# Kernel tuning notes

Hardware: AMD Instinct MI355X
Metric: run time of the kernel (lower is better)

The kernel has to match this reference:

```python
import jax, jax.numpy as jnp
import numpy as np
from jax import lax

NUM_CLASSES = 5
N_ITER = 3
IC = 32 * 14 * 14  # 6272 primary capsules
IN_DIM = 14
OUT_DIM = 1


def squash(s):
    # s: [B, N, D]; squash along capsule dim D (dim=2 in torch code)
    sq = jnp.sum(s * s, axis=2)
    scale = sq / (1.0 + sq) / jnp.sqrt(sq)
    return s * scale[:, :, None]


def setup_inputs() -> dict:
    key = jax.random.key(0)
    ks = jax.random.split(key, 7)
    B = 1024
    inp = jax.random.normal(ks[0], (B, 1, 59, 59), dtype=jnp.float32)
    # conv1: Conv2d(1, 32, k=5, s=2)
    W1 = jax.random.normal(ks[1], (32, 1, 5, 5), dtype=jnp.float32) * 0.1
    b1 = jax.random.normal(ks[2], (32,), dtype=jnp.float32) * 0.01
    # primary caps conv: Conv2d(32, 32*14, k=1, s=2) -> 1x1 kernel stored as [448,32]
    Wp = jax.random.normal(ks[3], (32 * 14, 32), dtype=jnp.float32) * 0.1
    bp = jax.random.normal(ks[4], (32 * 14,), dtype=jnp.float32) * 0.01
    # digit caps transform weights: [input_caps, input_dim, output_caps*output_dim]
    stdv = 1.0 / np.sqrt(IC)
    caps_W = jax.random.uniform(ks[5], (IC, IN_DIM, NUM_CLASSES * OUT_DIM), dtype=jnp.float32,
                                minval=-stdv, maxval=stdv)
    # routing logits (learned, initialized zero in torch)
    b_route = jnp.zeros((IC, NUM_CLASSES), dtype=jnp.float32)
    return {"input": inp, "r": 3, "W1": W1, "b1": b1, "Wp": Wp, "bp": bp,
            "caps_W": caps_W, "b_route": b_route}


def _forward(inp, W1, b1, Wp, bp, caps_W, b_route):
    B = inp.shape[0]
    # conv1 + relu: [B,32,28,28]
    x = lax.conv_general_dilated(inp, W1, window_strides=(2, 2), padding="VALID",
                                 dimension_numbers=("NCHW", "OIHW", "NCHW"))
    x = jax.nn.relu(x + b1[None, :, None, None])
    # primary caps: 1x1 conv with stride 2 == strided slice + channel matmul
    xs = x[:, :, ::2, ::2]  # [B,32,14,14]
    pc = jnp.einsum("oc,bchw->bohw", Wp, xs) + bp[None, :, None, None]  # [B,448,14,14]
    pc = pc.reshape(B, 32, 14, 14, 14)          # [B, caps, dim, H, W]
    pc = jnp.transpose(pc, (0, 1, 3, 4, 2))     # [B, caps, H, W, dim]
    pc = pc.reshape(B, IC, IN_DIM)              # [B, 6272, 14]
    pc = squash(pc)
    # digit caps predictions: u_predict [B, IC, OC, OD]
    u = jnp.einsum("bni,nio->bno", pc, caps_W).reshape(B, IC, NUM_CLASSES, OUT_DIM)
    # routing by agreement
    c = jax.nn.softmax(b_route, axis=1)                     # [IC, OC]
    s = jnp.einsum("io,biod->bod", c, u)                    # [B, OC, OD]
    v = squash(s)
    b_batch = jnp.broadcast_to(b_route, (B, IC, NUM_CLASSES))
    for _ in range(N_ITER):
        b_batch = b_batch + jnp.sum(u * v[:, None, :, :], axis=-1)
        c = jax.nn.softmax(b_batch, axis=2)                 # [B, IC, OC]
        s = jnp.einsum("bio,biod->bod", c, u)
        v = squash(s)
    # class probabilities = capsule lengths: [B, OC]
    return jnp.sqrt(jnp.sum(v * v, axis=2))


def reference(input, r, W1, b1, Wp, bp, caps_W, b_route):
    # r is accepted but unused, matching the torch forward signature
    return _forward(input, W1, b1, Wp, bp, caps_W, b_route)
```

## Files before the change

kernel.cpp:

```cpp
#include <hip/hip_runtime.h>
#include <math.h>


#define NTH    512
#define NWAVES 8
#define IC     6272
#define NCLS   5

__global__ __launch_bounds__(NTH, 1)
void caps_fused(const float* __restrict__ inp,
                const float* __restrict__ W1,
                const float* __restrict__ b1,
                const float* __restrict__ Wp,
                const float* __restrict__ bp,
                const float* __restrict__ capsW,
                const float* __restrict__ broute,
                float* __restrict__ out)
{
    extern __shared__ float lds[];
    float* s_xs  = lds;
    float* s_W1  = s_xs + 6272;
    float* s_b1  = s_W1 + 800;
    float* s_bp  = s_b1 + 32;
    float* s_red = s_bp + 448;
    float* s_v   = s_red + 40;
    float* s_u   = s_v + 8;
    float* s_in  = s_u;

    const int b    = blockIdx.x;
    const int tid  = threadIdx.x;
    const int lane = tid & 63;
    const int wv   = tid >> 6;

    const float* inb = inp + (size_t)b * (59 * 59);
    for (int i = tid; i < 59 * 59; i += NTH) s_in[i] = inb[i];
    for (int i = tid; i < 800;     i += NTH) s_W1[i] = W1[i];
    if (tid < 32) s_b1[tid] = b1[tid];
    for (int i = tid; i < 448;     i += NTH) s_bp[i] = bp[i];
    __syncthreads();

    for (int n = tid; n < IC; n += NTH) {
        const int c  = n / 196;
        const int hw = n - c * 196;
        const int h  = hw / 14;
        const int w  = hw - h * 14;
        const float* ip = s_in + (4 * h) * 59 + 4 * w;
        const float* wk = s_W1 + c * 25;
        float acc = s_b1[c];
        #pragma unroll
        for (int kh = 0; kh < 5; ++kh)
            #pragma unroll
            for (int kw = 0; kw < 5; ++kw)
                acc = fmaf(ip[kh * 59 + kw], wk[kh * 5 + kw], acc);
        s_xs[n] = fmaxf(acc, 0.0f);
    }
    __syncthreads();

    for (int gi = 0; gi < 4; ++gi) {
        const int g = wv + gi * NWAVES;
        float pc0[14], pc1[14], pc2[14], pc3[14];
        #pragma unroll
        for (int i = 0; i < 14; ++i) { pc0[i] = 0.f; pc1[i] = 0.f; pc2[i] = 0.f; pc3[i] = 0.f; }
        const float* wpg = Wp + (size_t)g * (14 * 32);
        for (int c = 0; c < 32; ++c) {
            const float* xc = s_xs + c * 196;
            const float x0 = xc[lane];
            const float x1 = xc[64 + lane];
            const float x2 = xc[128 + lane];
            const float x3 = xc[192 + (lane & 3)];
            #pragma unroll
            for (int i = 0; i < 14; ++i) {
                const float w = wpg[i * 32 + c];
                pc0[i] = fmaf(w, x0, pc0[i]);
                pc1[i] = fmaf(w, x1, pc1[i]);
                pc2[i] = fmaf(w, x2, pc2[i]);
                pc3[i] = fmaf(w, x3, pc3[i]);
            }
        }
        auto emit = [&](float* pc, int r) {
            const int hw = r * 64 + lane;
            if (hw < 196) {
                const int n = g * 196 + hw;
                float sq = 0.f;
                #pragma unroll
                for (int i = 0; i < 14; ++i) {
                    pc[i] += s_bp[g * 14 + i];
                    sq = fmaf(pc[i], pc[i], sq);
                }
                const float scale = sq / (1.0f + sq) / sqrtf(sq);
                float uo[5] = {0.f, 0.f, 0.f, 0.f, 0.f};
                const float* cw = capsW + (size_t)n * 70;
                #pragma unroll
                for (int i = 0; i < 14; ++i) {
                    const float p = pc[i] * scale;
                    #pragma unroll
                    for (int o = 0; o < 5; ++o)
                        uo[o] = fmaf(p, cw[i * 5 + o], uo[o]);
                }
                #pragma unroll
                for (int o = 0; o < 5; ++o) s_u[n * 5 + o] = uo[o];
            }
        };
        emit(pc0, 0); emit(pc1, 1); emit(pc2, 2); emit(pc3, 3);
    }
    __syncthreads();

    float V[5] = {0.f, 0.f, 0.f, 0.f, 0.f};
    for (int it = 0; it < 4; ++it) {
        float sacc[5] = {0.f, 0.f, 0.f, 0.f, 0.f};
        for (int n = tid; n < IC; n += NTH) {
            const float* br = broute + (size_t)n * 5;
            float uu[5], l[5];
            #pragma unroll
            for (int o = 0; o < 5; ++o) {
                uu[o] = s_u[n * 5 + o];
                l[o]  = fmaf(uu[o], V[o], br[o]);
            }
            const float m = fmaxf(fmaxf(fmaxf(l[0], l[1]), fmaxf(l[2], l[3])), l[4]);
            float e[5], es = 0.f;
            #pragma unroll
            for (int o = 0; o < 5; ++o) { e[o] = __expf(l[o] - m); es += e[o]; }
            const float inv = 1.0f / es;
            #pragma unroll
            for (int o = 0; o < 5; ++o)
                sacc[o] = fmaf(uu[o], e[o] * inv, sacc[o]);
        }
        #pragma unroll
        for (int off = 32; off > 0; off >>= 1)
            #pragma unroll
            for (int o = 0; o < 5; ++o)
                sacc[o] += __shfl_down(sacc[o], off);
        if (lane == 0) {
            #pragma unroll
            for (int o = 0; o < 5; ++o) s_red[wv * 5 + o] = sacc[o];
        }
        __syncthreads();
        if (tid == 0) {
            #pragma unroll
            for (int o = 0; o < 5; ++o) {
                float s = 0.f;
                for (int w2 = 0; w2 < NWAVES; ++w2) s += s_red[w2 * 5 + o];
                s_v[o] = s * fabsf(s) / (1.0f + s * s);
            }
        }
        __syncthreads();
        #pragma unroll
        for (int o = 0; o < 5; ++o) V[o] += s_v[o];
    }

    if (tid < NCLS) out[b * NCLS + tid] = fabsf(s_v[tid]);
}

extern "C" void kernel_launch(void* const* d_in, const int* in_sizes, int n_in,
                              void* d_out, int out_size, void* d_ws, size_t ws_size,
                              hipStream_t stream)
{
    const float* inp   = (const float*)d_in[0];
    const float* W1    = (const float*)d_in[2];
    const float* b1    = (const float*)d_in[3];
    const float* Wp    = (const float*)d_in[4];
    const float* bp    = (const float*)d_in[5];
    const float* capsW = (const float*)d_in[6];
    const float* brt   = (const float*)d_in[7];
    float* out = (float*)d_out;

    const int B = in_sizes[0] / (59 * 59);
    const size_t lds_bytes = (size_t)(6272 + 800 + 32 + 448 + 40 + 8 + 31360) * sizeof(float);
    (void)hipFuncSetAttribute((const void*)caps_fused,
                              hipFuncAttributeMaxDynamicSharedMemorySize,
                              (int)lds_bytes);
    caps_fused<<<B, NTH, lds_bytes, stream>>>(inp, W1, b1, Wp, bp, capsW, brt, out);
}
```

Measured before the change: 618.5 us.

## Keep capsule predictions in registers, stage Wp in LDS, double threads

Doubles the block to 1024 threads (16 waves) so each wave handles two capsule groups instead of four. The per-capsule prediction vectors u stay in registers across the routing iterations rather than going through a large LDS buffer. This shrinks LDS use from about 155KB to about 73KB, which could let more than one block share a CU. Wp slices are staged into LDS in a transposed layout instead of being read per lane from global memory, and the squash scale is simplified algebraically. The cost is heavier register pressure from holding 40 u values per thread at a 1024-thread launch bound, which risks spilling.

```diff
diff --git a/kernel.cpp b/kernel.cpp
--- a/kernel.cpp
+++ b/kernel.cpp
@@ -2,12 +2,12 @@
 #include <math.h>
 
 
-#define NTH    512
-#define NWAVES 8
+#define NTH    1024
+#define NW     16
 #define IC     6272
 #define NCLS   5
 
-__global__ __launch_bounds__(NTH, 1)
+__global__ __launch_bounds__(NTH)
 void caps_fused(const float* __restrict__ inp,
                 const float* __restrict__ W1,
                 const float* __restrict__ b1,
@@ -18,14 +18,14 @@
                 float* __restrict__ out)
 {
     extern __shared__ float lds[];
-    float* s_xs  = lds;
-    float* s_W1  = s_xs + 6272;
+    float* s_in  = lds;
+    float* s_W1  = s_in + 3481;
     float* s_b1  = s_W1 + 800;
     float* s_bp  = s_b1 + 32;
-    float* s_red = s_bp + 448;
-    float* s_v   = s_red + 40;
-    float* s_u   = s_v + 8;
-    float* s_in  = s_u;
+    float* s_xs  = s_bp + 448;
+    float* s_wp  = s_xs + 6272;
+    float* s_red = s_wp + 7168;
+    float* s_v   = s_red + 80;
 
     const int b    = blockIdx.x;
     const int tid  = threadIdx.x;
@@ -36,7 +36,7 @@
     for (int i = tid; i < 59 * 59; i += NTH) s_in[i] = inb[i];
     for (int i = tid; i < 800;     i += NTH) s_W1[i] = W1[i];
     if (tid < 32) s_b1[tid] = b1[tid];
-    for (int i = tid; i < 448;     i += NTH) s_bp[i] = bp[i];
+    if (tid < 448) s_bp[tid] = bp[tid];
     __syncthreads();
 
     for (int n = tid; n < IC; n += NTH) {
@@ -54,98 +54,120 @@
                 acc = fmaf(ip[kh * 59 + kw], wk[kh * 5 + kw], acc);
         s_xs[n] = fmaxf(acc, 0.0f);
     }
-    __syncthreads();
 
-    for (int gi = 0; gi < 4; ++gi) {
-        const int g = wv + gi * NWAVES;
+    float u[2][4][NCLS];
+
+    #pragma unroll
+    for (int gi = 0; gi < 2; ++gi) {
+        __syncthreads();
+        for (int idx = tid; idx < 16 * 448; idx += NTH) {
+            const int c     = idx & 31;
+            const int i     = (idx >> 5) % 14;
+            const int slice = idx / 448;
+            s_wp[slice * 448 + c * 14 + i] = Wp[(size_t)(slice + gi * 16) * 448 + i * 32 + c];
+        }
+        __syncthreads();
+
+        const int g = wv + gi * 16;
+        const float* wpb = s_wp + wv * 448;
         float pc0[14], pc1[14], pc2[14], pc3[14];
         #pragma unroll
-        for (int i = 0; i < 14; ++i) { pc0[i] = 0.f; pc1[i] = 0.f; pc2[i] = 0.f; pc3[i] = 0.f; }
-        const float* wpg = Wp + (size_t)g * (14 * 32);
+        for (int i = 0; i < 14; ++i) {
+            const float bias = s_bp[g * 14 + i];
+            pc0[i] = bias; pc1[i] = bias; pc2[i] = bias; pc3[i] = bias;
+        }
         for (int c = 0; c < 32; ++c) {
             const float* xc = s_xs + c * 196;
             const float x0 = xc[lane];
             const float x1 = xc[64 + lane];
             const float x2 = xc[128 + lane];
             const float x3 = xc[192 + (lane & 3)];
+            const float* wc = wpb + c * 14;
             #pragma unroll
             for (int i = 0; i < 14; ++i) {
-                const float w = wpg[i * 32 + c];
+                const float w = wc[i];
                 pc0[i] = fmaf(w, x0, pc0[i]);
                 pc1[i] = fmaf(w, x1, pc1[i]);
                 pc2[i] = fmaf(w, x2, pc2[i]);
                 pc3[i] = fmaf(w, x3, pc3[i]);
             }
         }
-        auto emit = [&](float* pc, int r) {
-            const int hw = r * 64 + lane;
-            if (hw < 196) {
-                const int n = g * 196 + hw;
-                float sq = 0.f;
-                #pragma unroll
-                for (int i = 0; i < 14; ++i) {
-                    pc[i] += s_bp[g * 14 + i];
-                    sq = fmaf(pc[i], pc[i], sq);
-                }
-                const float scale = sq / (1.0f + sq) / sqrtf(sq);
-                float uo[5] = {0.f, 0.f, 0.f, 0.f, 0.f};
-                const float* cw = capsW + (size_t)n * 70;
-                #pragma unroll
-                for (int i = 0; i < 14; ++i) {
-                    const float p = pc[i] * scale;
-                    #pragma unroll
-                    for (int o = 0; o < 5; ++o)
-                        uo[o] = fmaf(p, cw[i * 5 + o], uo[o]);
-                }
-                #pragma unroll
-                for (int o = 0; o < 5; ++o) s_u[n * 5 + o] = uo[o];
-            }
-        };
-        emit(pc0, 0); emit(pc1, 1); emit(pc2, 2); emit(pc3, 3);
+
+        #define EMIT(PC, R)                                                     \
+        {                                                                       \
+            const int hw = (R) * 64 + lane;                                     \
+            if (hw < 196) {                                                     \
+                const int n = g * 196 + hw;                                     \
+                float sq = 0.f;                                                 \
+                _Pragma("unroll")                                               \
+                for (int i = 0; i < 14; ++i) sq = fmaf(PC[i], PC[i], sq);       \
+                const float scale = sqrtf(sq) / (1.0f + sq);                    \
+                float uo[NCLS] = {0.f, 0.f, 0.f, 0.f, 0.f};                     \
+                const float* cw = capsW + (size_t)n * 70;                       \
+                _Pragma("unroll")                                               \
+                for (int i = 0; i < 14; ++i) {                                  \
+                    const float p = PC[i] * scale;                              \
+                    _Pragma("unroll")                                           \
+                    for (int o = 0; o < NCLS; ++o)                              \
+                        uo[o] = fmaf(p, cw[i * 5 + o], uo[o]);                  \
+                }                                                               \
+                _Pragma("unroll")                                               \
+                for (int o = 0; o < NCLS; ++o) u[gi][R][o] = uo[o];             \
+            } else {                                                            \
+                _Pragma("unroll")                                               \
+                for (int o = 0; o < NCLS; ++o) u[gi][R][o] = 0.f;               \
+            }                                                                   \
+        }
+        EMIT(pc0, 0) EMIT(pc1, 1) EMIT(pc2, 2) EMIT(pc3, 3)
+        #undef EMIT
     }
     __syncthreads();
 
-    float V[5] = {0.f, 0.f, 0.f, 0.f, 0.f};
+    float V[NCLS] = {0.f, 0.f, 0.f, 0.f, 0.f};
     for (int it = 0; it < 4; ++it) {
-        float sacc[5] = {0.f, 0.f, 0.f, 0.f, 0.f};
-        for (int n = tid; n < IC; n += NTH) {
-            const float* br = broute + (size_t)n * 5;
-            float uu[5], l[5];
+        float sacc[NCLS] = {0.f, 0.f, 0.f, 0.f, 0.f};
+        #pragma unroll
+        for (int gi = 0; gi < 2; ++gi) {
+            const int g = wv + gi * 16;
             #pragma unroll
-            for (int o = 0; o < 5; ++o) {
-                uu[o] = s_u[n * 5 + o];
-                l[o]  = fmaf(uu[o], V[o], br[o]);
+            for (int r = 0; r < 4; ++r) {
+                const int hw = r * 64 + lane;
+                if (hw < 196) {
+                    const int n = g * 196 + hw;
+                    const float* br = broute + (size_t)n * 5;
+                    float l[NCLS];
+                    #pragma unroll
+                    for (int o = 0; o < NCLS; ++o)
+                        l[o] = fmaf(u[gi][r][o], V[o], br[o]);
+                    const float m = fmaxf(fmaxf(fmaxf(l[0], l[1]), fmaxf(l[2], l[3])), l[4]);
+                    float e[NCLS], es = 0.f;
+                    #pragma unroll
+                    for (int o = 0; o < NCLS; ++o) { e[o] = __expf(l[o] - m); es += e[o]; }
+                    const float inv = 1.0f / es;
+                    #pragma unroll
+                    for (int o = 0; o < NCLS; ++o)
+                        sacc[o] = fmaf(u[gi][r][o], e[o] * inv, sacc[o]);
+                }
             }
-            const float m = fmaxf(fmaxf(fmaxf(l[0], l[1]), fmaxf(l[2], l[3])), l[4]);
-            float e[5], es = 0.f;
-            #pragma unroll
-            for (int o = 0; o < 5; ++o) { e[o] = __expf(l[o] - m); es += e[o]; }
-            const float inv = 1.0f / es;
-            #pragma unroll
-            for (int o = 0; o < 5; ++o)
-                sacc[o] = fmaf(uu[o], e[o] * inv, sacc[o]);
         }
         #pragma unroll
         for (int off = 32; off > 0; off >>= 1)
             #pragma unroll
-            for (int o = 0; o < 5; ++o)
+            for (int o = 0; o < NCLS; ++o)
                 sacc[o] += __shfl_down(sacc[o], off);
         if (lane == 0) {
             #pragma unroll
-            for (int o = 0; o < 5; ++o) s_red[wv * 5 + o] = sacc[o];
+            for (int o = 0; o < NCLS; ++o) s_red[wv * 5 + o] = sacc[o];
         }
         __syncthreads();
-        if (tid == 0) {
-            #pragma unroll
-            for (int o = 0; o < 5; ++o) {
-                float s = 0.f;
-                for (int w2 = 0; w2 < NWAVES; ++w2) s += s_red[w2 * 5 + o];
-                s_v[o] = s * fabsf(s) / (1.0f + s * s);
-            }
+        if (tid < NCLS) {
+            float s = 0.f;
+            for (int w2 = 0; w2 < NW; ++w2) s += s_red[w2 * 5 + tid];
+            s_v[tid] = s * fabsf(s) / (1.0f + s * s);
         }
         __syncthreads();
         #pragma unroll
-        for (int o = 0; o < 5; ++o) V[o] += s_v[o];
+        for (int o = 0; o < NCLS; ++o) V[o] += s_v[o];
     }
 
     if (tid < NCLS) out[b * NCLS + tid] = fabsf(s_v[tid]);
@@ -165,7 +187,7 @@
     float* out = (float*)d_out;
 
     const int B = in_sizes[0] / (59 * 59);
-    const size_t lds_bytes = (size_t)(6272 + 800 + 32 + 448 + 40 + 8 + 31360) * sizeof(float);
+    const size_t lds_bytes = (size_t)(3481 + 800 + 32 + 448 + 6272 + 7168 + 80 + 8) * sizeof(float);
     (void)hipFuncSetAttribute((const void*)caps_fused,
                               hipFuncAttributeMaxDynamicSharedMemorySize,
                               (int)lds_bytes);
```

Result: slower. 1.573 ms (+154.3%).

## Transpose xs to swizzled HW-major layout and vectorize primary-caps matmul loads

Applied to the files above, without the earlier changes.

Stores the conv1 output as [hw][32 channels] with an XOR swizzle so each lane can load all 32 channels for its position with float4 LDS reads without bank conflicts. The primary-caps matmul now loops over positions in pairs, holding 32 inputs in registers, and reads Wp and bias with a wave-uniform (readfirstlane) base so they can become scalar loads. It also drops the LDS bias copy and simplifies the squash scale to sqrt(sq)/(1+sq). This aims to cut LDS traffic and per-channel global weight loads, but raises register pressure (64 input values plus 28 accumulators) and could cause spills.

```diff
diff --git a/kernel.cpp b/kernel.cpp
--- a/kernel.cpp
+++ b/kernel.cpp
@@ -21,8 +21,7 @@
     float* s_xs  = lds;
     float* s_W1  = s_xs + 6272;
     float* s_b1  = s_W1 + 800;
-    float* s_bp  = s_b1 + 32;
-    float* s_red = s_bp + 448;
+    float* s_red = s_b1 + 32;
     float* s_v   = s_red + 40;
     float* s_u   = s_v + 8;
     float* s_in  = s_u;
@@ -31,12 +30,12 @@
     const int tid  = threadIdx.x;
     const int lane = tid & 63;
     const int wv   = tid >> 6;
+    const int wvs  = __builtin_amdgcn_readfirstlane(wv);
 
     const float* inb = inp + (size_t)b * (59 * 59);
     for (int i = tid; i < 59 * 59; i += NTH) s_in[i] = inb[i];
     for (int i = tid; i < 800;     i += NTH) s_W1[i] = W1[i];
     if (tid < 32) s_b1[tid] = b1[tid];
-    for (int i = tid; i < 448;     i += NTH) s_bp[i] = bp[i];
     __syncthreads();
 
     for (int n = tid; n < IC; n += NTH) {
@@ -52,92 +51,109 @@
             #pragma unroll
             for (int kw = 0; kw < 5; ++kw)
                 acc = fmaf(ip[kh * 59 + kw], wk[kh * 5 + kw], acc);
-        s_xs[n] = fmaxf(acc, 0.0f);
+        const int col = 4 * ((c >> 2) ^ (hw & 7)) + (c & 3);
+        s_xs[hw * 32 + col] = fmaxf(acc, 0.0f);
     }
     __syncthreads();
 
+    const float4* xs4 = (const float4*)s_xs;
+
+    #define EMIT(PC, HW)                                                    \
+    {                                                                       \
+        if ((HW) < 196) {                                                   \
+            const int n = g * 196 + (HW);                                   \
+            float sq = 0.f;                                                 \
+            _Pragma("unroll")                                               \
+            for (int i = 0; i < 14; ++i) sq = fmaf(PC[i], PC[i], sq);       \
+            const float scale = sqrtf(sq) / (1.0f + sq);                    \
+            float uo[NCLS] = {0.f, 0.f, 0.f, 0.f, 0.f};                     \
+            const float* cw = capsW + (size_t)n * 70;                       \
+            _Pragma("unroll")                                               \
+            for (int i = 0; i < 14; ++i) {                                  \
+                const float p = PC[i] * scale;                              \
+                _Pragma("unroll")                                           \
+                for (int o = 0; o < NCLS; ++o)                              \
+                    uo[o] = fmaf(p, cw[i * 5 + o], uo[o]);                  \
+            }                                                               \
+            _Pragma("unroll")                                               \
+            for (int o = 0; o < NCLS; ++o) s_u[n * 5 + o] = uo[o];          \
+        }                                                                   \
+    }
+
     for (int gi = 0; gi < 4; ++gi) {
-        const int g = wv + gi * NWAVES;
-        float pc0[14], pc1[14], pc2[14], pc3[14];
+        const int g = wvs + gi * 8;
+        const float* wpg = Wp + g * 448;
+        const float* bpg = bp + g * 14;
+
         #pragma unroll
-        for (int i = 0; i < 14; ++i) { pc0[i] = 0.f; pc1[i] = 0.f; pc2[i] = 0.f; pc3[i] = 0.f; }
-        const float* wpg = Wp + (size_t)g * (14 * 32);
-        for (int c = 0; c < 32; ++c) {
-            const float* xc = s_xs + c * 196;
-            const float x0 = xc[lane];
-            const float x1 = xc[64 + lane];
-            const float x2 = xc[128 + lane];
-            const float x3 = xc[192 + (lane & 3)];
+        for (int p = 0; p < 2; ++p) {
+            const int hwA = p * 128 + lane;
+            const int hwB = p ? (192 + (lane & 3)) : (64 + lane);
+            float xA[32], xB[32];
+            #pragma unroll
+            for (int j = 0; j < 8; ++j) {
+                const float4 a  = xs4[hwA * 8 + (j ^ (hwA & 7))];
+                const float4 bb = xs4[hwB * 8 + (j ^ (hwB & 7))];
+                xA[4*j+0] = a.x;  xA[4*j+1] = a.y;  xA[4*j+2] = a.z;  xA[4*j+3] = a.w;
+                xB[4*j+0] = bb.x; xB[4*j+1] = bb.y; xB[4*j+2] = bb.z; xB[4*j+3] = bb.w;
+            }
+
+            float pcA[14], pcB[14];
             #pragma unroll
             for (int i = 0; i < 14; ++i) {
-                const float w = wpg[i * 32 + c];
-                pc0[i] = fmaf(w, x0, pc0[i]);
-                pc1[i] = fmaf(w, x1, pc1[i]);
-                pc2[i] = fmaf(w, x2, pc2[i]);
-                pc3[i] = fmaf(w, x3, pc3[i]);
+                const float bias = bpg[i];
+                pcA[i] = bias; pcB[i] = bias;
             }
+            #pragma unroll
+            for (int i = 0; i < 14; ++i) {
+                const float* wr = wpg + i * 32;
+                #pragma unroll
+                for (int c = 0; c < 32; ++c) {
+                    const float w = wr[c];
+                    pcA[i] = fmaf(w, xA[c], pcA[i]);
+                    pcB[i] = fmaf(w, xB[c], pcB[i]);
+                }
+            }
+            EMIT(pcA, hwA)
+            EMIT(pcB, hwB)
         }
-        auto emit = [&](float* pc, int r) {
-            const int hw = r * 64 + lane;
-            if (hw < 196) {
-                const int n = g * 196 + hw;
-                float sq = 0.f;
-                #pragma unroll
-                for (int i = 0; i < 14; ++i) {
-                    pc[i] += s_bp[g * 14 + i];
-                    sq = fmaf(pc[i], pc[i], sq);
-                }
-                const float scale = sq / (1.0f + sq) / sqrtf(sq);
-                float uo[5] = {0.f, 0.f, 0.f, 0.f, 0.f};
-                const float* cw = capsW + (size_t)n * 70;
-                #pragma unroll
-                for (int i = 0; i < 14; ++i) {
-                    const float p = pc[i] * scale;
-                    #pragma unroll
-                    for (int o = 0; o < 5; ++o)
-                        uo[o] = fmaf(p, cw[i * 5 + o], uo[o]);
-                }
-                #pragma unroll
-                for (int o = 0; o < 5; ++o) s_u[n * 5 + o] = uo[o];
-            }
-        };
-        emit(pc0, 0); emit(pc1, 1); emit(pc2, 2); emit(pc3, 3);
     }
+    #undef EMIT
     __syncthreads();
 
-    float V[5] = {0.f, 0.f, 0.f, 0.f, 0.f};
+    float V[NCLS] = {0.f, 0.f, 0.f, 0.f, 0.f};
     for (int it = 0; it < 4; ++it) {
-        float sacc[5] = {0.f, 0.f, 0.f, 0.f, 0.f};
+        float sacc[NCLS] = {0.f, 0.f, 0.f, 0.f, 0.f};
         for (int n = tid; n < IC; n += NTH) {
             const float* br = broute + (size_t)n * 5;
-            float uu[5], l[5];
+            float uu[NCLS], l[NCLS];
             #pragma unroll
-            for (int o = 0; o < 5; ++o) {
+            for (int o = 0; o < NCLS; ++o) {
                 uu[o] = s_u[n * 5 + o];
                 l[o]  = fmaf(uu[o], V[o], br[o]);
             }
             const float m = fmaxf(fmaxf(fmaxf(l[0], l[1]), fmaxf(l[2], l[3])), l[4]);
-            float e[5], es = 0.f;
+            float e[NCLS], es = 0.f;
             #pragma unroll
-            for (int o = 0; o < 5; ++o) { e[o] = __expf(l[o] - m); es += e[o]; }
+            for (int o = 0; o < NCLS; ++o) { e[o] = __expf(l[o] - m); es += e[o]; }
             const float inv = 1.0f / es;
             #pragma unroll
-            for (int o = 0; o < 5; ++o)
+            for (int o = 0; o < NCLS; ++o)
                 sacc[o] = fmaf(uu[o], e[o] * inv, sacc[o]);
         }
         #pragma unroll
         for (int off = 32; off > 0; off >>= 1)
             #pragma unroll
-            for (int o = 0; o < 5; ++o)
+            for (int o = 0; o < NCLS; ++o)
                 sacc[o] += __shfl_down(sacc[o], off);
         if (lane == 0) {
             #pragma unroll
-            for (int o = 0; o < 5; ++o) s_red[wv * 5 + o] = sacc[o];
+            for (int o = 0; o < NCLS; ++o) s_red[wv * 5 + o] = sacc[o];
         }
         __syncthreads();
         if (tid == 0) {
             #pragma unroll
-            for (int o = 0; o < 5; ++o) {
+            for (int o = 0; o < NCLS; ++o) {
                 float s = 0.f;
                 for (int w2 = 0; w2 < NWAVES; ++w2) s += s_red[w2 * 5 + o];
                 s_v[o] = s * fabsf(s) / (1.0f + s * s);
@@ -145,7 +161,7 @@
         }
         __syncthreads();
         #pragma unroll
-        for (int o = 0; o < 5; ++o) V[o] += s_v[o];
+        for (int o = 0; o < NCLS; ++o) V[o] += s_v[o];
     }
 
     if (tid < NCLS) out[b * NCLS + tid] = fabsf(s_v[tid]);
@@ -165,7 +181,7 @@
     float* out = (float*)d_out;
 
     const int B = in_sizes[0] / (59 * 59);
-    const size_t lds_bytes = (size_t)(6272 + 800 + 32 + 448 + 40 + 8 + 31360) * sizeof(float);
+    const size_t lds_bytes = (size_t)(6272 + 800 + 32 + 40 + 8 + 31360) * sizeof(float);
     (void)hipFuncSetAttribute((const void*)caps_fused,
                               hipFuncAttributeMaxDynamicSharedMemorySize,
                               (int)lds_bytes);
```

After: 686.9 us. 11.0% more time.
